# Optimization experiments

Measured on AMD Instinct MI355X. Metric: run time of the kernel, lower is better.

## Reference

```python
import jax, jax.numpy as jnp
import numpy as np

THRESHOLD = 0.5
EPS = 1e-6


def setup_inputs() -> dict:
    key = jax.random.key(0)
    k1, k2, k3 = jax.random.split(key, 3)
    B, C, T = 32, 6, 64
    K, N = 8, 128
    S, P = 32, 64
    points = jax.random.normal(k1, (B, C, T, 2), dtype=jnp.float32)
    road_boundary = jax.random.normal(k2, (B, K, N, 2), dtype=jnp.float32)
    centerlines = jax.random.normal(k3, (B, S, P, 2), dtype=jnp.float32)
    return {"points": points, "road_boundary": road_boundary, "centerlines": centerlines}


def _cross(v1, v2):
    return v1[..., 0] * v2[..., 1] - v1[..., 1] * v2[..., 0]


def reference(points, road_boundary, centerlines):
    B, C, T, _ = points.shape
    _, K, N, _ = road_boundary.shape
    _, S, P, _ = centerlines.shape

    # --- min distance to boundary segments ---
    seg_a = road_boundary[:, :, :-1, :]          # (B,K,N-1,2)
    seg_d = road_boundary[:, :, 1:, :] - seg_a   # (B,K,N-1,2)

    p = points[:, None, :, :, None, :]           # (B,1,C,T,1,2)
    a = seg_a[:, :, None, None, :, :]            # (B,K,1,1,N-1,2)
    d = seg_d[:, :, None, None, :, :]            # (B,K,1,1,N-1,2)

    v1 = p - a                                   # (B,K,C,T,N-1,2)
    dot = (v1 * d).sum(-1)                       # (B,K,C,T,N-1)
    edge_sq = (d * d).sum(-1)                    # (B,K,1,1,N-1)
    proj = jnp.clip(dot / (edge_sq + EPS), 0.0, 1.0)
    closest = a + d * proj[..., None]            # (B,K,C,T,N-1,2)
    dist = jnp.sqrt(((p - closest) ** 2).sum(-1))  # (B,K,C,T,N-1)
    min_dist = dist.min(axis=-1).min(axis=1)     # (B,C,T)

    # --- nearest centerline point ---
    cl = centerlines.reshape(B, S * P, 2)        # (B,SP,2)
    v2 = points[:, None, :, :, :] - cl[:, :, None, None, :]  # (B,SP,C,T,2)
    cl_dist_sq = (v2 ** 2).sum(-1)               # (B,SP,C,T)
    idx = jnp.argmin(cl_dist_sq, axis=1)         # (B,C,T)
    closest_cl = cl[jnp.arange(B)[:, None, None], idx]  # (B,C,T,2)

    # --- segment intersection test: (point -> nearest centerline pt) vs boundary edges ---
    a1 = points[:, None, None, :, :, :]          # (B,1,1,C,T,2)
    a2 = closest_cl[:, None, None, :, :, :]      # (B,1,1,C,T,2)
    b1 = seg_a[:, :, :, None, None, :]           # (B,K,N-1,1,1,2)
    db = seg_d[:, :, :, None, None, :]           # (B,K,N-1,1,1,2)

    da = a2 - a1
    dp = a1 - b1                                 # (B,K,N-1,C,T,2)
    dadb = _cross(da, db)                        # (B,K,N-1,C,T)
    t = _cross(da, dp) / (dadb + EPS)
    u = _cross(db, dp) / (dadb + EPS)
    intersect = (t >= 0.0) & (t <= 1.0) & (u >= 0.0) & (u <= 1.0)

    inside = ~jnp.any(intersect, axis=(1, 2))    # (B,C,T)
    min_dist = jnp.where(inside, -min_dist, min_dist)
    return jax.nn.relu(min_dist + THRESHOLD).sum(-1)  # (B,C)
```

## Files before the change

### kernel.cpp

```cpp
#include <hip/hip_runtime.h>

constexpr int cB = 32, cC = 6, cT = 64;
constexpr int cK = 8, cN = 128;
constexpr int cS = 32, cP = 64;
constexpr int NSEG = cK * (cN - 1);
constexpr int NSEG_PAD = 1024;
constexpr int NCL  = cS * cP;
constexpr int G = 4;
constexpr int LPP = 16;
constexpr float F_EPS = 1e-6f;
constexpr float F_THRESHOLD = 0.5f;

__global__ __launch_bounds__(256) void offroad_kernel(
    const float* __restrict__ points,
    const float* __restrict__ road_boundary,
    const float* __restrict__ centerlines,
    float* __restrict__ out)
{
    __shared__ float4 s_seg[NSEG_PAD];
    __shared__ float  s_inv[NSEG_PAD];
    __shared__ float4 s_cl4[NCL / 2];
    __shared__ float  s_part[4];

    const int blk = blockIdx.x;
    const int g  = blk & (G - 1);
    const int bc = blk >> 2;
    const int b  = bc / cC;
    const int tid = threadIdx.x;

    const float* rb = road_boundary + (size_t)b * cK * cN * 2;
    for (int s = tid; s < NSEG_PAD; s += 256) {
        if (s < NSEG) {
            int k = s / (cN - 1);
            int n = s - k * (cN - 1);
            const float* p0 = rb + (k * cN + n) * 2;
            float ax = p0[0], ay = p0[1];
            float dx = p0[2] - ax, dy = p0[3] - ay;
            s_seg[s] = make_float4(ax, ay, dx, dy);
            s_inv[s] = 1.0f / (dx * dx + dy * dy + F_EPS);
        } else {
            s_seg[s] = make_float4(1e18f, 1e18f, 0.0f, 0.0f);
            s_inv[s] = 0.0f;
        }
    }
    const float4* cl4 = (const float4*)(centerlines + (size_t)b * NCL * 2);
    for (int i = tid; i < NCL / 2; i += 256) s_cl4[i] = cl4[i];
    __syncthreads();

    const int t = (g << 4) | (tid >> 4);
    const int q = tid & (LPP - 1);
    const size_t pbase = (((size_t)bc) * cT + t) * 2;
    const float px = points[pbase + 0];
    const float py = points[pbase + 1];

    float min_d2 = 3.4e38f;
    #pragma unroll 4
    for (int s = q; s < NSEG_PAD; s += LPP) {
        float4 sg = s_seg[s];
        float v1x = px - sg.x, v1y = py - sg.y;
        float dot = v1x * sg.z + v1y * sg.w;
        float proj = dot * s_inv[s];
        proj = fminf(fmaxf(proj, 0.0f), 1.0f);
        float ex = v1x - sg.z * proj;
        float ey = v1y - sg.w * proj;
        float d2 = ex * ex + ey * ey;
        min_d2 = fminf(min_d2, d2);
    }

    float best_d2 = 3.4e38f;
    int best_i = 0x7fffffff;
    #pragma unroll 4
    for (int j = q; j < NCL / 2; j += LPP) {
        float4 cp = s_cl4[j];
        float dxa = px - cp.x, dya = py - cp.y;
        float d2a = dxa * dxa + dya * dya;
        float dxb = px - cp.z, dyb = py - cp.w;
        float d2b = dxb * dxb + dyb * dyb;
        int   ia = 2 * j;
        float dmin = d2a; int imin = ia;
        if (d2b < d2a) { dmin = d2b; imin = ia + 1; }
        if (dmin < best_d2 || (dmin == best_d2 && imin < best_i)) {
            best_d2 = dmin; best_i = imin;
        }
    }
    #pragma unroll
    for (int off = 1; off <= 8; off <<= 1) {
        float od2 = __shfl_xor(best_d2, off);
        int   oi  = __shfl_xor(best_i, off);
        if (od2 < best_d2 || (od2 == best_d2 && oi < best_i)) {
            best_d2 = od2; best_i = oi;
        }
    }
    const float2* s_cl2 = (const float2*)s_cl4;
    const float2 cc = s_cl2[best_i];

    const float dax = cc.x - px, day = cc.y - py;
    int hit = 0;
    #pragma unroll 4
    for (int s = q; s < NSEG_PAD; s += LPP) {
        float4 sg = s_seg[s];
        float dpx = px - sg.x, dpy = py - sg.y;
        float dadb = dax * sg.w - day * sg.z;
        float inv = 1.0f / (dadb + F_EPS);
        float tt = (dax * dpy - day * dpx) * inv;
        float uu = (sg.z * dpy - sg.w * dpx) * inv;
        bool inb = (tt >= 0.0f) & (tt <= 1.0f) & (uu >= 0.0f) & (uu <= 1.0f);
        hit |= (int)((s < NSEG) & inb);
    }

    #pragma unroll
    for (int off = 1; off <= 8; off <<= 1) {
        min_d2 = fminf(min_d2, __shfl_xor(min_d2, off));
        hit |= __shfl_xor(hit, off);
    }

    float md = sqrtf(min_d2);
    float sd = hit ? md : -md;
    float val = fmaxf(sd + F_THRESHOLD, 0.0f);
    if (q != 0) val = 0.0f;

    #pragma unroll
    for (int off = 32; off >= 1; off >>= 1)
        val += __shfl_down(val, off);
    const int wave = tid >> 6;
    if ((tid & 63) == 0) s_part[wave] = val;
    __syncthreads();
    if (tid == 0)
        atomicAdd(&out[bc], s_part[0] + s_part[1] + s_part[2] + s_part[3]);
}

extern "C" void kernel_launch(void* const* d_in, const int* in_sizes, int n_in,
                              void* d_out, int out_size, void* d_ws, size_t ws_size,
                              hipStream_t stream) {
    const float* points      = (const float*)d_in[0];
    const float* boundary    = (const float*)d_in[1];
    const float* centerlines = (const float*)d_in[2];
    float* out = (float*)d_out;
    hipMemsetAsync(out, 0, (size_t)out_size * sizeof(float), stream);
    offroad_kernel<<<cB * cC * G, 256, 0, stream>>>(points, boundary, centerlines, out);
}
```

Measured before the change: 86.32 us.

## Double blocks per batch row, fuse distance loops, pad segments with NaN

Doubles the grid to eight blocks per (b,c), with 32 lanes per point instead of 16. Segments keep their natural K×N layout, and pad slots are filled with NaN so invalid entries drop out of the min and intersection tests without index checks. The boundary-distance and centerline-argmin loops are merged, and inverse edge lengths are computed in-loop with the hardware reciprocal instead of being stored in shared memory. The final per-block shared reduction and barrier are replaced by one atomicAdd per wave. The trade-offs are more redundant shared-memory staging per block, more atomics, and approximate reciprocals, which can change results near the boundaries.

```diff
diff --git a/kernel.cpp b/kernel.cpp
--- a/kernel.cpp
+++ b/kernel.cpp
@@ -3,11 +3,10 @@
 constexpr int cB = 32, cC = 6, cT = 64;
 constexpr int cK = 8, cN = 128;
 constexpr int cS = 32, cP = 64;
-constexpr int NSEG = cK * (cN - 1);
-constexpr int NSEG_PAD = 1024;
+constexpr int NSEG_PAD = cK * cN;
 constexpr int NCL  = cS * cP;
-constexpr int G = 4;
-constexpr int LPP = 16;
+constexpr int G = 8;
+constexpr int LPP = 32;
 constexpr float F_EPS = 1e-6f;
 constexpr float F_THRESHOLD = 0.5f;
 
@@ -18,59 +17,55 @@
     float* __restrict__ out)
 {
     __shared__ float4 s_seg[NSEG_PAD];
-    __shared__ float  s_inv[NSEG_PAD];
     __shared__ float4 s_cl4[NCL / 2];
-    __shared__ float  s_part[4];
 
     const int blk = blockIdx.x;
     const int g  = blk & (G - 1);
-    const int bc = blk >> 2;
+    const int bc = blk >> 3;
     const int b  = bc / cC;
     const int tid = threadIdx.x;
 
-    const float* rb = road_boundary + (size_t)b * cK * cN * 2;
+    const float qnan = __int_as_float(0x7fc00000);
+
+    const float2* rb2 = (const float2*)(road_boundary + (size_t)b * cK * cN * 2);
     for (int s = tid; s < NSEG_PAD; s += 256) {
-        if (s < NSEG) {
-            int k = s / (cN - 1);
-            int n = s - k * (cN - 1);
-            const float* p0 = rb + (k * cN + n) * 2;
-            float ax = p0[0], ay = p0[1];
-            float dx = p0[2] - ax, dy = p0[3] - ay;
-            s_seg[s] = make_float4(ax, ay, dx, dy);
-            s_inv[s] = 1.0f / (dx * dx + dy * dy + F_EPS);
+        int n = s & (cN - 1);
+        if (n < cN - 1) {
+            float2 a  = rb2[s];
+            float2 nx = rb2[s + 1];
+            s_seg[s] = make_float4(a.x, a.y, nx.x - a.x, nx.y - a.y);
         } else {
-            s_seg[s] = make_float4(1e18f, 1e18f, 0.0f, 0.0f);
-            s_inv[s] = 0.0f;
+            s_seg[s] = make_float4(qnan, qnan, qnan, qnan);
         }
     }
     const float4* cl4 = (const float4*)(centerlines + (size_t)b * NCL * 2);
     for (int i = tid; i < NCL / 2; i += 256) s_cl4[i] = cl4[i];
     __syncthreads();
 
-    const int t = (g << 4) | (tid >> 4);
+    const int t = (g << 3) | (tid >> 5);
     const int q = tid & (LPP - 1);
     const size_t pbase = (((size_t)bc) * cT + t) * 2;
     const float px = points[pbase + 0];
     const float py = points[pbase + 1];
 
     float min_d2 = 3.4e38f;
+    float best_d2 = 3.4e38f;
+    int best_i = 0x7fffffff;
     #pragma unroll 4
-    for (int s = q; s < NSEG_PAD; s += LPP) {
+    for (int i = 0; i < NSEG_PAD / LPP; ++i) {
+        int s = q + i * LPP;
         float4 sg = s_seg[s];
         float v1x = px - sg.x, v1y = py - sg.y;
         float dot = v1x * sg.z + v1y * sg.w;
-        float proj = dot * s_inv[s];
+        float e2  = sg.z * sg.z + sg.w * sg.w + F_EPS;
+        float proj = dot * __builtin_amdgcn_rcpf(e2);
         proj = fminf(fmaxf(proj, 0.0f), 1.0f);
         float ex = v1x - sg.z * proj;
         float ey = v1y - sg.w * proj;
         float d2 = ex * ex + ey * ey;
         min_d2 = fminf(min_d2, d2);
-    }
 
-    float best_d2 = 3.4e38f;
-    int best_i = 0x7fffffff;
-    #pragma unroll 4
-    for (int j = q; j < NCL / 2; j += LPP) {
+        int j = q + i * LPP;
         float4 cp = s_cl4[j];
         float dxa = px - cp.x, dya = py - cp.y;
         float d2a = dxa * dxa + dya * dya;
@@ -84,7 +79,7 @@
         }
     }
     #pragma unroll
-    for (int off = 1; off <= 8; off <<= 1) {
+    for (int off = 1; off <= 16; off <<= 1) {
         float od2 = __shfl_xor(best_d2, off);
         int   oi  = __shfl_xor(best_i, off);
         if (od2 < best_d2 || (od2 == best_d2 && oi < best_i)) {
@@ -97,19 +92,19 @@
     const float dax = cc.x - px, day = cc.y - py;
     int hit = 0;
     #pragma unroll 4
-    for (int s = q; s < NSEG_PAD; s += LPP) {
+    for (int i = 0; i < NSEG_PAD / LPP; ++i) {
+        int s = q + i * LPP;
         float4 sg = s_seg[s];
         float dpx = px - sg.x, dpy = py - sg.y;
         float dadb = dax * sg.w - day * sg.z;
-        float inv = 1.0f / (dadb + F_EPS);
+        float inv = __builtin_amdgcn_rcpf(dadb + F_EPS);
         float tt = (dax * dpy - day * dpx) * inv;
         float uu = (sg.z * dpy - sg.w * dpx) * inv;
-        bool inb = (tt >= 0.0f) & (tt <= 1.0f) & (uu >= 0.0f) & (uu <= 1.0f);
-        hit |= (int)((s < NSEG) & inb);
+        hit |= (tt >= 0.0f && tt <= 1.0f && uu >= 0.0f && uu <= 1.0f) ? 1 : 0;
     }
 
     #pragma unroll
-    for (int off = 1; off <= 8; off <<= 1) {
+    for (int off = 1; off <= 16; off <<= 1) {
         min_d2 = fminf(min_d2, __shfl_xor(min_d2, off));
         hit |= __shfl_xor(hit, off);
     }
@@ -122,11 +117,8 @@
     #pragma unroll
     for (int off = 32; off >= 1; off >>= 1)
         val += __shfl_down(val, off);
-    const int wave = tid >> 6;
-    if ((tid & 63) == 0) s_part[wave] = val;
-    __syncthreads();
-    if (tid == 0)
-        atomicAdd(&out[bc], s_part[0] + s_part[1] + s_part[2] + s_part[3]);
+    if ((tid & 63) == 0)
+        atomicAdd(&out[bc], val);
 }
 
 extern "C" void kernel_launch(void* const* d_in, const int* in_sizes, int n_in,
```

Result: slower. 99.42 us (+15.2%).
